# Performance work log

Measured on AMD Instinct MI355X. Metric: run time of the kernel, lower is better.

## Reference

```python
import jax, jax.numpy as jnp
import numpy as np

B, C, H, W = 2, 1024, 64, 64
E, TOP_K = 8, 2
FFN = C  # ffn_dim = in_channels; hidden_dim = out_channels = in_channels


def setup_inputs() -> dict:
    key = jax.random.key(0)
    ks = jax.random.split(key, 5)
    s = 0.02
    return {
        "hidden_states": jax.random.normal(ks[0], (B, C, H, W), jnp.float32),
        "gate_w": jax.random.normal(ks[1], (E, C), jnp.float32) * s,   # torch Linear weight [out,in]
        "w1": jax.random.normal(ks[2], (E, FFN, C), jnp.float32) * s,
        "w2": jax.random.normal(ks[3], (E, C, FFN), jnp.float32) * s,
        "w3": jax.random.normal(ks[4], (E, FFN, C), jnp.float32) * s,
    }


def reference(hidden_states, gate_w, w1, w2, w3):
    b, c = hidden_states.shape[0], hidden_states.shape[1]
    space = hidden_states.shape[2:]
    # (B, C, H, W) -> (B, H, W, C) -> (T, C)
    x = jnp.transpose(hidden_states, (0, 2, 3, 1)).reshape(-1, c)

    # Router: softmax in float32, top-k, renormalize (matches torch)
    logits = x @ gate_w.T                                   # [T, E]
    probs = jax.nn.softmax(logits.astype(jnp.float32), axis=-1)
    rw, sel = jax.lax.top_k(probs, TOP_K)                   # [T, K]
    rw = rw / jnp.sum(rw, axis=-1, keepdims=True)
    rw = rw.astype(x.dtype)

    # Combine weights per expert: zero where expert not selected -> exact
    # equivalence with gather/scatter dispatch (full capacity, no drops).
    combine = jnp.sum(jax.nn.one_hot(sel, E, dtype=x.dtype) * rw[..., None], axis=1)  # [T, E]

    out = jnp.zeros_like(x)
    for e in range(E):  # small fixed expert loop
        h = jax.nn.gelu(x @ w1[e].T, approximate=False) * (x @ w3[e].T)  # SwiGLU-style [T, FFN]
        out = out + combine[:, e:e + 1] * (h @ w2[e].T)

    out = out.reshape(b, *space, c)
    return jnp.transpose(out, (0, 3, 1, 2))  # (B, C, H, W)
```

## Files before the change

### kernel.cpp

```cpp
#include <hip/hip_runtime.h>
#include <hip/hip_bf16.h>
#include <math.h>

#define BB 2
#define CC 1024
#define HH 64
#define WW 64
#define HWH (HH*WW)
#define TT (BB*HWH)
#define EE 8
#define FFN 1024
#define MAXTILES 71
#define HCAP (MAXTILES*256)

typedef __bf16 bf16x8 __attribute__((ext_vector_type(8)));
typedef float  f32x4  __attribute__((ext_vector_type(4)));

__device__ __forceinline__ void gl_lds16(const __bf16* g, __bf16* l) {
    __builtin_amdgcn_global_load_lds(
        (const __attribute__((address_space(1))) void*)g,
        (__attribute__((address_space(3))) void*)l, 16, 0, 0);
}

__device__ __forceinline__ void barrier_raw() {
    asm volatile("" ::: "memory");
    __builtin_amdgcn_s_barrier();
    asm volatile("" ::: "memory");
}

__device__ __forceinline__ int xcd_swz(int orig, int nwg) {
    const int q = nwg >> 3, r = nwg & 7, x = orig & 7, o8 = orig >> 3;
    return (x < r ? x * (q + 1) : r * (q + 1) + (x - r) * q) + o8;
}

__device__ __forceinline__ float gelu_fast(float a) {
    const float a2 = a * a;
    const float t  = a * fmaf(0.044715f, a2, 1.0f);
    const float u  = __builtin_amdgcn_exp2f(t * -2.30220795f);
    return a * __builtin_amdgcn_rcpf(1.0f + u);
}

#define WAITV(N) asm volatile("s_waitcnt vmcnt(" #N ")" ::: "memory")
#define LGKM0()  asm volatile("s_waitcnt lgkmcnt(0)" ::: "memory")
#define SCHED0() __builtin_amdgcn_sched_barrier(0)
#define PRIO1()  __builtin_amdgcn_s_setprio(1)
#define PRIO0()  __builtin_amdgcn_s_setprio(0)

#define CVB 12288
#define XPB 8192
#define RTB 512
__global__ __launch_bounds__(256) void k_prep(
    const float* __restrict__ hs, const float* __restrict__ gate_w,
    const float* __restrict__ w1, const float* __restrict__ w2,
    const float* __restrict__ w3,
    __bf16* __restrict__ w1b, __bf16* __restrict__ w2b,
    __bf16* __restrict__ w3b, __bf16* __restrict__ X,
    float* __restrict__ logP) {
    __shared__ float sm[2112];
    const int bid = blockIdx.x;
    const int tid = threadIdx.x;

    if (bid < CVB) {
        const float* s; __bf16* d; int lb = bid;
        if (lb < 4096)      { s = w1; d = w1b; }
        else if (lb < 8192) { s = w2; d = w2b; lb -= 4096; }
        else                { s = w3; d = w3b; lb -= 8192; }
        const size_t i = (size_t)lb * 2048 + (size_t)tid * 8;
        const f32x4 v0 = *(const f32x4*)&s[i];
        const f32x4 v1 = *(const f32x4*)&s[i + 4];
        bf16x8 o;
#pragma unroll
        for (int j = 0; j < 4; ++j) { o[j] = (__bf16)v0[j]; o[4 + j] = (__bf16)v1[j]; }
        *(bf16x8*)&d[i] = o;
    } else if (bid < CVB + XPB) {
        const int lb  = bid - CVB;
        const int hw0 = (lb & 127) * 32;
        const int c0  = ((lb >> 7) & 31) * 32;
        const int b   = lb >> 12;
        float (*tile)[33] = (float(*)[33])sm;
        const int tx = tid & 31, ty = tid >> 5;
        const float* src = hs + ((size_t)b * CC + c0) * HWH + hw0;
#pragma unroll
        for (int i = 0; i < 4; ++i)
            tile[ty + i * 8][tx] = src[(size_t)(ty + i * 8) * HWH + tx];
        __syncthreads();
        __bf16* dst = X + ((size_t)b * HWH + hw0) * CC + c0;
#pragma unroll
        for (int i = 0; i < 4; ++i) {
            const int hwl = ty + i * 8;
            dst[(size_t)hwl * CC + tx] = (__bf16)tile[tx][hwl];
        }
    } else {
        const int lb  = bid - (CVB + XPB);
        const int q   = lb & 3;
        const int t64 = lb >> 2;
        float* g = sm;
        for (int i = tid; i < 2048; i += 256)
            g[i] = gate_w[(size_t)(i >> 8) * CC + q * 256 + (i & 255)];
        __syncthreads();
        const int q2 = tid >> 6, tl = tid & 63;
        const int t  = t64 * 64 + tl;
        const int b  = t >> 12, hw = t & 4095;
        const float* xp = hs + (size_t)b * CC * HWH + hw;
        float l[EE];
#pragma unroll
        for (int e = 0; e < EE; ++e) l[e] = 0.0f;
        const int cbase = q * 256 + q2 * 64;
        for (int c2 = 0; c2 < 64; ++c2) {
            const float xv = xp[(size_t)(cbase + c2) * HWH];
#pragma unroll
            for (int e = 0; e < EE; ++e) l[e] += xv * g[e * 256 + q2 * 64 + c2];
        }
        float* dst = logP + ((size_t)(q * 4 + q2) * TT + t) * 8;
        f32x4 a, c;
#pragma unroll
        for (int e = 0; e < 4; ++e) { a[e] = l[e]; c[e] = l[4 + e]; }
        *(f32x4*)dst = a;
        *(f32x4*)&dst[4] = c;
    }
}

__global__ __launch_bounds__(256) void k_top2(const float* __restrict__ logP,
                                              int* __restrict__ cnt,
                                              int* __restrict__ idxl,
                                              int* __restrict__ tokE,
                                              int* __restrict__ tokP,
                                              float* __restrict__ tokW) {
    __shared__ int lcnt[EE], lbase[EE];
    const int tid = threadIdx.x;
    const int t   = blockIdx.x * 256 + tid;
    if (tid < EE) lcnt[tid] = 0;
    __syncthreads();

    float l[EE];
#pragma unroll
    for (int e = 0; e < EE; ++e) l[e] = 0.0f;
#pragma unroll
    for (int pq = 0; pq < 16; ++pq) {
        const float* src = logP + ((size_t)pq * TT + t) * 8;
        const f32x4 a = *(const f32x4*)src;
        const f32x4 c = *(const f32x4*)&src[4];
#pragma unroll
        for (int e = 0; e < 4; ++e) { l[e] += a[e]; l[4 + e] += c[e]; }
    }

    int e1 = 0; float v1 = l[0];
#pragma unroll
    for (int e = 1; e < EE; ++e) { if (l[e] > v1) { v1 = l[e]; e1 = e; } }
    int e2 = -1; float v2 = -1e30f;
#pragma unroll
    for (int e = 0; e < EE; ++e) { if (e != e1 && l[e] > v2) { v2 = l[e]; e2 = e; } }

    const float p2 = __expf(v2 - v1);
    const float rs = 1.0f / (1.0f + p2);

    const int m1 = atomicAdd(&lcnt[e1], 1);
    const int m2 = atomicAdd(&lcnt[e2], 1);
    __syncthreads();
    if (tid < EE) lbase[tid] = atomicAdd(&cnt[tid], lcnt[tid]);
    __syncthreads();
    const int p1pos = lbase[e1] + m1;
    const int p2pos = lbase[e2] + m2;

    idxl[e1 * TT + p1pos] = t;
    idxl[e2 * TT + p2pos] = t;
    tokE[t] = e1 | (e2 << 8);
    tokP[2 * t]     = p1pos;
    tokP[2 * t + 1] = p2pos;
    tokW[2 * t]     = rs;
    tokW[2 * t + 1] = p2 * rs;
}

#define GT_TILE(SR, SS, KB, STG, WC) do {                                     \
    if (STG) {                                                                \
        gl_lds16(gA0 + (KB), &sA[SS][stA]);                                   \
        gl_lds16(gA1 + (KB), &sA[SS][stA + 4096]);                            \
        gl_lds16(gB0 + (KB), &sB[SS][stA]);                                   \
    }                                                                         \
    bf16x8 af[4], bv[4];                                                      \
    _Pragma("unroll") for (int f_ = 0; f_ < 4; ++f_) {                        \
        af[f_] = *(const bf16x8*)&sA[SR][aoff + f_ * 512];                    \
        bv[f_] = *(const bf16x8*)&sB[SR][boff + f_ * 512];                    \
    }                                                                         \
    LGKM0(); SCHED0();                                                        \
    PRIO1();                                                                  \
    _Pragma("unroll") for (int m_ = 0; m_ < 4; ++m_)                          \
    _Pragma("unroll") for (int n_ = 0; n_ < 4; ++n_)                          \
        acc[m_][n_] = __builtin_amdgcn_mfma_f32_16x16x32_bf16(                \
            af[m_], bv[n_], acc[m_][n_], 0, 0, 0);                            \
    PRIO0();                                                                  \
    WC;                                                                       \
    barrier_raw();                                                            \
} while (0)

__global__ __launch_bounds__(512, 4)
void k_gemm1(const __bf16* __restrict__ X, const __bf16* __restrict__ w1b,
             const __bf16* __restrict__ w3b, const int* __restrict__ cnt,
             const int* __restrict__ idxl, __bf16* __restrict__ H) {
    const int lid = blockIdx.y * 16 + blockIdx.x;
    const int wg  = xcd_swz(lid, 16 * MAXTILES);
    const int n0  = (wg & 15) * 64;
    int ty = wg >> 4;
    int e = -1, mt = 0, goff = 0, acc_rows = 0;
#pragma unroll
    for (int ee = 0; ee < EE; ++ee) {
        const int me = (cnt[ee] + 255) >> 8;
        if (ty >= 0 && ty < me) { e = ee; mt = ty << 8; goff = acc_rows; }
        ty -= me;
        acc_rows += me << 8;
    }
    if (e < 0) return;
    const int cntE = cnt[e];
    const __bf16* W1 = w1b + (size_t)e * FFN * CC;
    const __bf16* W3 = w3b + (size_t)e * FFN * CC;

    __shared__ __align__(16) __bf16 sA[3][8192];
    __shared__ __align__(16) __bf16 sB[3][4096];

    const int tid  = threadIdx.x;
    const int lane = tid & 63, wave = tid >> 6;
    const int l15  = lane & 15, lq = lane >> 4;
    const int wm   = wave & 3;
    const int wq   = wave >> 2;
    const int rsw  = (lq ^ ((l15 >> 1) & 3)) * 8;

    const int csw  = ((tid & 3) ^ ((tid >> 3) & 3)) * 8;
    const int cswb = ((lane & 3) ^ ((lane >> 3) & 3)) * 8;

    int pr0 = mt + (tid >> 2);        if (pr0 > cntE - 1) pr0 = cntE - 1;
    int pr1 = mt + 128 + (tid >> 2);  if (pr1 > cntE - 1) pr1 = cntE - 1;
    const __bf16* gA0 = X + (size_t)idxl[e * TT + pr0] * CC + csw;
    const __bf16* gA1 = X + (size_t)idxl[e * TT + pr1] * CC + csw;
    const __bf16* WB  = (wave & 1) ? W3 : W1;
    const __bf16* gB0 = WB + (size_t)(n0 + (wave >> 1) * 16 + (lane >> 2)) * CC + cswb;

    const int stA  = wave * 512;
    const int aoff = (wm * 64 + l15) * 32 + rsw;
    const int boff = (wq * 64 + l15) * 32 + rsw;

    f32x4 acc[4][4] = {};

    gl_lds16(gA0,      &sA[0][stA]); gl_lds16(gA1,      &sA[0][stA + 4096]);
    gl_lds16(gB0,      &sB[0][stA]);
    gl_lds16(gA0 + 32, &sA[1][stA]); gl_lds16(gA1 + 32, &sA[1][stA + 4096]);
    gl_lds16(gB0 + 32, &sB[1][stA]);
    WAITV(3);
    barrier_raw();

    int kb = 64;
    for (int it = 0; it < 10; ++it) {
        GT_TILE(0, 2, kb, 1, WAITV(3)); kb += 32;
        GT_TILE(1, 0, kb, 1, WAITV(3)); kb += 32;
        GT_TILE(2, 1, kb, 1, WAITV(3)); kb += 32;
    }
    GT_TILE(0, 0, 0, 0, WAITV(0));
    GT_TILE(1, 0, 0, 0, (void)0);

#pragma unroll
    for (int mf = 0; mf < 4; ++mf) {
        const int gr  = goff + mt + wm * 64 + mf * 16 + lq * 4;
        const int col = n0 + wq * 32 + l15;
#pragma unroll
        for (int r = 0; r < 4; ++r) {
            const float a0 = acc[mf][0][r], c0 = acc[mf][1][r];
            const float a1 = acc[mf][2][r], c1 = acc[mf][3][r];
            H[(size_t)(gr + r) * FFN + col]      = (__bf16)(gelu_fast(a0) * c0);
            H[(size_t)(gr + r) * FFN + col + 16] = (__bf16)(gelu_fast(a1) * c1);
        }
    }
}

__global__ __launch_bounds__(512, 4)
void k_gemm2(const __bf16* __restrict__ H, const __bf16* __restrict__ w2b,
             const int* __restrict__ cnt, __bf16* __restrict__ Z) {
    const int lid = blockIdx.y * 8 + blockIdx.x;
    const int wg  = xcd_swz(lid, 8 * MAXTILES);
    const int n0  = (wg & 7) * 128;
    int ty = wg >> 3;
    int e = -1, mt = 0, goff = 0, acc_rows = 0;
#pragma unroll
    for (int ee = 0; ee < EE; ++ee) {
        const int me = (cnt[ee] + 255) >> 8;
        if (ty >= 0 && ty < me) { e = ee; mt = ty << 8; goff = acc_rows; }
        ty -= me;
        acc_rows += me << 8;
    }
    if (e < 0) return;
    const __bf16* W2 = w2b + (size_t)e * CC * FFN;
    const __bf16* Ar = H + (size_t)(goff + mt) * FFN;

    __shared__ __align__(16) __bf16 sA[3][8192];
    __shared__ __align__(16) __bf16 sB[3][4096];

    const int tid  = threadIdx.x;
    const int lane = tid & 63, wave = tid >> 6;
    const int l15  = lane & 15, lq = lane >> 4;
    const int wm   = wave & 3;
    const int wq   = wave >> 2;
    const int rsw  = (lq ^ ((l15 >> 1) & 3)) * 8;
    const int csw  = ((tid & 3) ^ ((tid >> 3) & 3)) * 8;
    const int cswb = ((lane & 3) ^ ((lane >> 3) & 3)) * 8;

    const __bf16* gA0 = Ar + (size_t)(tid >> 2) * FFN + csw;
    const __bf16* gA1 = Ar + (size_t)(128 + (tid >> 2)) * FFN + csw;
    const __bf16* gB0 = W2 + (size_t)(n0 + wave * 16 + (lane >> 2)) * FFN + cswb;

    const int stA  = wave * 512;
    const int aoff = (wm * 64 + l15) * 32 + rsw;
    const int boff = (wq * 64 + l15) * 32 + rsw;

    f32x4 acc[4][4] = {};

    gl_lds16(gA0,      &sA[0][stA]); gl_lds16(gA1,      &sA[0][stA + 4096]);
    gl_lds16(gB0,      &sB[0][stA]);
    gl_lds16(gA0 + 32, &sA[1][stA]); gl_lds16(gA1 + 32, &sA[1][stA + 4096]);
    gl_lds16(gB0 + 32, &sB[1][stA]);
    WAITV(3);
    barrier_raw();

    int kb = 64;
    for (int it = 0; it < 10; ++it) {
        GT_TILE(0, 2, kb, 1, WAITV(3)); kb += 32;
        GT_TILE(1, 0, kb, 1, WAITV(3)); kb += 32;
        GT_TILE(2, 1, kb, 1, WAITV(3)); kb += 32;
    }
    GT_TILE(0, 0, 0, 0, WAITV(0));
    GT_TILE(1, 0, 0, 0, (void)0);

#pragma unroll
    for (int mf = 0; mf < 4; ++mf) {
        const int gr = goff + mt + wm * 64 + mf * 16 + lq * 4;
#pragma unroll
        for (int nf = 0; nf < 4; ++nf) {
            const int col = n0 + wq * 64 + nf * 16 + l15;
#pragma unroll
            for (int r = 0; r < 4; ++r)
                Z[(size_t)(gr + r) * CC + col] = (__bf16)acc[mf][nf][r];
        }
    }
}

__global__ __launch_bounds__(256) void k_combine(const __bf16* __restrict__ Z,
                                                 const int* __restrict__ cnt,
                                                 const int* __restrict__ tokE,
                                                 const int* __restrict__ tokP,
                                                 const float* __restrict__ tokW,
                                                 float* __restrict__ out) {
    __shared__ float tile[32][33];
    __shared__ int s_pre[EE];
    const int tid = threadIdx.x;
    if (tid < EE) {
        int a = 0;
        for (int ee = 0; ee < tid; ++ee) a += ((cnt[ee] + 255) >> 8) << 8;
        s_pre[tid] = a;
    }
    __syncthreads();

    const int t0 = blockIdx.x * 32;
    const int c0 = blockIdx.y * 32;
    const int tx = tid & 31;
    const int ty = tid >> 5;

#pragma unroll
    for (int i = 0; i < 4; ++i) {
        const int tl = ty + 8 * i;
        const int t  = t0 + tl;
        const int ee = tokE[t];
        const int e1 = ee & 0xff, e2 = ee >> 8;
        const int r1 = s_pre[e1] + tokP[2 * t];
        const int r2 = s_pre[e2] + tokP[2 * t + 1];
        const float v = tokW[2 * t]     * (float)Z[(size_t)r1 * CC + c0 + tx]
                      + tokW[2 * t + 1] * (float)Z[(size_t)r2 * CC + c0 + tx];
        tile[tl][tx] = v;
    }
    __syncthreads();

    const int b   = t0 >> 12;
    const int hw0 = t0 & 4095;
#pragma unroll
    for (int i = 0; i < 4; ++i) {
        const int cl = ty + 8 * i;
        out[(size_t)b * CC * HWH + (size_t)(c0 + cl) * HWH + hw0 + tx] = tile[tx][cl];
    }
}

extern "C" void kernel_launch(void* const* d_in, const int* in_sizes, int n_in,
                              void* d_out, int out_size, void* d_ws, size_t ws_size,
                              hipStream_t stream) {
    const float* hs     = (const float*)d_in[0];
    const float* gate_w = (const float*)d_in[1];
    const float* w1     = (const float*)d_in[2];
    const float* w2     = (const float*)d_in[3];
    const float* w3     = (const float*)d_in[4];
    float* out = (float*)d_out;

    const size_t WSZ = (size_t)EE * FFN * CC * 2;
    char* ws = (char*)d_ws;
    __bf16* w2b  = (__bf16*)ws;
    __bf16* w1b  = (__bf16*)(ws + WSZ);
    __bf16* w3b  = (__bf16*)(ws + 2 * WSZ);
    __bf16* X    = (__bf16*)(ws + 3 * WSZ);
    __bf16* Zbuf = (__bf16*)(ws + WSZ);
    __bf16* Hbuf = (__bf16*)(ws + 4 * WSZ);
    float*  logP = (float*)Hbuf;
    char* p = ws + 4 * WSZ + (size_t)HCAP * FFN * 2;
    int*   idxl  = (int*)p;           p += (size_t)EE * TT * 4;
    int*   tokE  = (int*)p;           p += (size_t)TT * 4;
    int*   tokP  = (int*)p;           p += (size_t)2 * TT * 4;
    float* tokW  = (float*)p;         p += (size_t)2 * TT * 4;
    int*   cnt   = (int*)p;           p += 256;

    hipMemsetAsync(cnt, 0, EE * sizeof(int), stream);

    k_prep<<<CVB + XPB + RTB, 256, 0, stream>>>(
        hs, gate_w, w1, w2, w3, w1b, w2b, w3b, X, logP);
    k_top2<<<TT / 256, 256, 0, stream>>>(logP, cnt, idxl, tokE, tokP, tokW);

    k_gemm1<<<dim3(FFN / 64, MAXTILES), 512, 0, stream>>>(
        X, w1b, w3b, cnt, idxl, Hbuf);
    k_gemm2<<<dim3(CC / 128, MAXTILES), 512, 0, stream>>>(
        Hbuf, w2b, cnt, Zbuf);
    k_combine<<<dim3(TT / 32, CC / 32), 256, 0, stream>>>(
        Zbuf, cnt, tokE, tokP, tokW, out);
}
```

Before: 329.8 us.

## Make expert GEMM kernels persistent with an atomic work-queue tile scheduler

Both grouped GEMM kernels now launch a fixed 512 workgroups. Each workgroup repeatedly pulls a tile index from a global atomic counter until all valid (expert, row-tile, column-tile) items are consumed. This replaces the oversized static grid with its XCD swizzle and early-exit blocks, aiming to remove empty launches and balance the tail. The cost is one atomic plus a block barrier per tile and the loss of the deliberate XCD-aware weight locality. Two extra counter slots are zeroed by the existing memset.

```diff
diff --git a/kernel.cpp b/kernel.cpp
--- a/kernel.cpp
+++ b/kernel.cpp
@@ -26,11 +26,6 @@
     asm volatile("" ::: "memory");
     __builtin_amdgcn_s_barrier();
     asm volatile("" ::: "memory");
-}
-
-__device__ __forceinline__ int xcd_swz(int orig, int nwg) {
-    const int q = nwg >> 3, r = nwg & 7, x = orig & 7, o8 = orig >> 3;
-    return (x < r ? x * (q + 1) : r * (q + 1) + (x - r) * q) + o8;
 }
 
 __device__ __forceinline__ float gelu_fast(float a) {
@@ -196,146 +191,165 @@
 __global__ __launch_bounds__(512, 4)
 void k_gemm1(const __bf16* __restrict__ X, const __bf16* __restrict__ w1b,
              const __bf16* __restrict__ w3b, const int* __restrict__ cnt,
-             const int* __restrict__ idxl, __bf16* __restrict__ H) {
-    const int lid = blockIdx.y * 16 + blockIdx.x;
-    const int wg  = xcd_swz(lid, 16 * MAXTILES);
-    const int n0  = (wg & 15) * 64;
-    int ty = wg >> 4;
-    int e = -1, mt = 0, goff = 0, acc_rows = 0;
-#pragma unroll
-    for (int ee = 0; ee < EE; ++ee) {
-        const int me = (cnt[ee] + 255) >> 8;
-        if (ty >= 0 && ty < me) { e = ee; mt = ty << 8; goff = acc_rows; }
-        ty -= me;
-        acc_rows += me << 8;
-    }
-    if (e < 0) return;
-    const int cntE = cnt[e];
-    const __bf16* W1 = w1b + (size_t)e * FFN * CC;
-    const __bf16* W3 = w3b + (size_t)e * FFN * CC;
-
+             const int* __restrict__ idxl, __bf16* __restrict__ H,
+             int* __restrict__ wq) {
     __shared__ __align__(16) __bf16 sA[3][8192];
     __shared__ __align__(16) __bf16 sB[3][4096];
+    __shared__ int s_item;
 
     const int tid  = threadIdx.x;
     const int lane = tid & 63, wave = tid >> 6;
     const int l15  = lane & 15, lq = lane >> 4;
     const int wm   = wave & 3;
-    const int wq   = wave >> 2;
+    const int wq_  = wave >> 2;
     const int rsw  = (lq ^ ((l15 >> 1) & 3)) * 8;
-
     const int csw  = ((tid & 3) ^ ((tid >> 3) & 3)) * 8;
     const int cswb = ((lane & 3) ^ ((lane >> 3) & 3)) * 8;
-
-    int pr0 = mt + (tid >> 2);        if (pr0 > cntE - 1) pr0 = cntE - 1;
-    int pr1 = mt + 128 + (tid >> 2);  if (pr1 > cntE - 1) pr1 = cntE - 1;
-    const __bf16* gA0 = X + (size_t)idxl[e * TT + pr0] * CC + csw;
-    const __bf16* gA1 = X + (size_t)idxl[e * TT + pr1] * CC + csw;
-    const __bf16* WB  = (wave & 1) ? W3 : W1;
-    const __bf16* gB0 = WB + (size_t)(n0 + (wave >> 1) * 16 + (lane >> 2)) * CC + cswb;
-
     const int stA  = wave * 512;
     const int aoff = (wm * 64 + l15) * 32 + rsw;
-    const int boff = (wq * 64 + l15) * 32 + rsw;
-
-    f32x4 acc[4][4] = {};
-
-    gl_lds16(gA0,      &sA[0][stA]); gl_lds16(gA1,      &sA[0][stA + 4096]);
-    gl_lds16(gB0,      &sB[0][stA]);
-    gl_lds16(gA0 + 32, &sA[1][stA]); gl_lds16(gA1 + 32, &sA[1][stA + 4096]);
-    gl_lds16(gB0 + 32, &sB[1][stA]);
-    WAITV(3);
-    barrier_raw();
-
-    int kb = 64;
-    for (int it = 0; it < 10; ++it) {
-        GT_TILE(0, 2, kb, 1, WAITV(3)); kb += 32;
-        GT_TILE(1, 0, kb, 1, WAITV(3)); kb += 32;
-        GT_TILE(2, 1, kb, 1, WAITV(3)); kb += 32;
-    }
-    GT_TILE(0, 0, 0, 0, WAITV(0));
-    GT_TILE(1, 0, 0, 0, (void)0);
-
-#pragma unroll
-    for (int mf = 0; mf < 4; ++mf) {
-        const int gr  = goff + mt + wm * 64 + mf * 16 + lq * 4;
-        const int col = n0 + wq * 32 + l15;
-#pragma unroll
-        for (int r = 0; r < 4; ++r) {
-            const float a0 = acc[mf][0][r], c0 = acc[mf][1][r];
-            const float a1 = acc[mf][2][r], c1 = acc[mf][3][r];
-            H[(size_t)(gr + r) * FFN + col]      = (__bf16)(gelu_fast(a0) * c0);
-            H[(size_t)(gr + r) * FFN + col + 16] = (__bf16)(gelu_fast(a1) * c1);
+    const int boff = (wq_ * 64 + l15) * 32 + rsw;
+
+    int nT = 0;
+#pragma unroll
+    for (int ee = 0; ee < EE; ++ee) nT += (cnt[ee] + 255) >> 8;
+    const int nItems = nT * 16;
+
+    for (;;) {
+        if (tid == 0) s_item = atomicAdd(wq, 1);
+        __syncthreads();
+        const int wg = s_item;
+        if (wg >= nItems) break;
+
+        const int n0 = (wg & 15) * 64;
+        int ty = wg >> 4;
+        int e = 0, mt = 0, goff = 0, acc_rows = 0;
+#pragma unroll
+        for (int ee = 0; ee < EE; ++ee) {
+            const int me = (cnt[ee] + 255) >> 8;
+            if (ty >= 0 && ty < me) { e = ee; mt = ty << 8; goff = acc_rows; }
+            ty -= me;
+            acc_rows += me << 8;
+        }
+        const int cntE = cnt[e];
+        const __bf16* W1 = w1b + (size_t)e * FFN * CC;
+        const __bf16* W3 = w3b + (size_t)e * FFN * CC;
+
+        int pr0 = mt + (tid >> 2);        if (pr0 > cntE - 1) pr0 = cntE - 1;
+        int pr1 = mt + 128 + (tid >> 2);  if (pr1 > cntE - 1) pr1 = cntE - 1;
+        const __bf16* gA0 = X + (size_t)idxl[e * TT + pr0] * CC + csw;
+        const __bf16* gA1 = X + (size_t)idxl[e * TT + pr1] * CC + csw;
+        const __bf16* WB  = (wave & 1) ? W3 : W1;
+        const __bf16* gB0 = WB + (size_t)(n0 + (wave >> 1) * 16 + (lane >> 2)) * CC + cswb;
+
+        f32x4 acc[4][4] = {};
+
+        gl_lds16(gA0,      &sA[0][stA]); gl_lds16(gA1,      &sA[0][stA + 4096]);
+        gl_lds16(gB0,      &sB[0][stA]);
+        gl_lds16(gA0 + 32, &sA[1][stA]); gl_lds16(gA1 + 32, &sA[1][stA + 4096]);
+        gl_lds16(gB0 + 32, &sB[1][stA]);
+        WAITV(3);
+        barrier_raw();
+
+        int kb = 64;
+        for (int it = 0; it < 10; ++it) {
+            GT_TILE(0, 2, kb, 1, WAITV(3)); kb += 32;
+            GT_TILE(1, 0, kb, 1, WAITV(3)); kb += 32;
+            GT_TILE(2, 1, kb, 1, WAITV(3)); kb += 32;
+        }
+        GT_TILE(0, 0, 0, 0, WAITV(0));
+        GT_TILE(1, 0, 0, 0, (void)0);
+
+#pragma unroll
+        for (int mf = 0; mf < 4; ++mf) {
+            const int gr  = goff + mt + wm * 64 + mf * 16 + lq * 4;
+            const int col = n0 + wq_ * 32 + l15;
+#pragma unroll
+            for (int r = 0; r < 4; ++r) {
+                const float a0 = acc[mf][0][r], c0 = acc[mf][1][r];
+                const float a1 = acc[mf][2][r], c1 = acc[mf][3][r];
+                H[(size_t)(gr + r) * FFN + col]      = (__bf16)(gelu_fast(a0) * c0);
+                H[(size_t)(gr + r) * FFN + col + 16] = (__bf16)(gelu_fast(a1) * c1);
+            }
         }
     }
 }
 
 __global__ __launch_bounds__(512, 4)
 void k_gemm2(const __bf16* __restrict__ H, const __bf16* __restrict__ w2b,
-             const int* __restrict__ cnt, __bf16* __restrict__ Z) {
-    const int lid = blockIdx.y * 8 + blockIdx.x;
-    const int wg  = xcd_swz(lid, 8 * MAXTILES);
-    const int n0  = (wg & 7) * 128;
-    int ty = wg >> 3;
-    int e = -1, mt = 0, goff = 0, acc_rows = 0;
-#pragma unroll
-    for (int ee = 0; ee < EE; ++ee) {
-        const int me = (cnt[ee] + 255) >> 8;
-        if (ty >= 0 && ty < me) { e = ee; mt = ty << 8; goff = acc_rows; }
-        ty -= me;
-        acc_rows += me << 8;
-    }
-    if (e < 0) return;
-    const __bf16* W2 = w2b + (size_t)e * CC * FFN;
-    const __bf16* Ar = H + (size_t)(goff + mt) * FFN;
-
+             const int* __restrict__ cnt, __bf16* __restrict__ Z,
+             int* __restrict__ wq) {
     __shared__ __align__(16) __bf16 sA[3][8192];
     __shared__ __align__(16) __bf16 sB[3][4096];
+    __shared__ int s_item;
 
     const int tid  = threadIdx.x;
     const int lane = tid & 63, wave = tid >> 6;
     const int l15  = lane & 15, lq = lane >> 4;
     const int wm   = wave & 3;
-    const int wq   = wave >> 2;
+    const int wq_  = wave >> 2;
     const int rsw  = (lq ^ ((l15 >> 1) & 3)) * 8;
     const int csw  = ((tid & 3) ^ ((tid >> 3) & 3)) * 8;
     const int cswb = ((lane & 3) ^ ((lane >> 3) & 3)) * 8;
-
-    const __bf16* gA0 = Ar + (size_t)(tid >> 2) * FFN + csw;
-    const __bf16* gA1 = Ar + (size_t)(128 + (tid >> 2)) * FFN + csw;
-    const __bf16* gB0 = W2 + (size_t)(n0 + wave * 16 + (lane >> 2)) * FFN + cswb;
-
     const int stA  = wave * 512;
     const int aoff = (wm * 64 + l15) * 32 + rsw;
-    const int boff = (wq * 64 + l15) * 32 + rsw;
-
-    f32x4 acc[4][4] = {};
-
-    gl_lds16(gA0,      &sA[0][stA]); gl_lds16(gA1,      &sA[0][stA + 4096]);
-    gl_lds16(gB0,      &sB[0][stA]);
-    gl_lds16(gA0 + 32, &sA[1][stA]); gl_lds16(gA1 + 32, &sA[1][stA + 4096]);
-    gl_lds16(gB0 + 32, &sB[1][stA]);
-    WAITV(3);
-    barrier_raw();
-
-    int kb = 64;
-    for (int it = 0; it < 10; ++it) {
-        GT_TILE(0, 2, kb, 1, WAITV(3)); kb += 32;
-        GT_TILE(1, 0, kb, 1, WAITV(3)); kb += 32;
-        GT_TILE(2, 1, kb, 1, WAITV(3)); kb += 32;
-    }
-    GT_TILE(0, 0, 0, 0, WAITV(0));
-    GT_TILE(1, 0, 0, 0, (void)0);
-
-#pragma unroll
-    for (int mf = 0; mf < 4; ++mf) {
-        const int gr = goff + mt + wm * 64 + mf * 16 + lq * 4;
-#pragma unroll
-        for (int nf = 0; nf < 4; ++nf) {
-            const int col = n0 + wq * 64 + nf * 16 + l15;
-#pragma unroll
-            for (int r = 0; r < 4; ++r)
-                Z[(size_t)(gr + r) * CC + col] = (__bf16)acc[mf][nf][r];
+    const int boff = (wq_ * 64 + l15) * 32 + rsw;
+
+    int nT = 0;
+#pragma unroll
+    for (int ee = 0; ee < EE; ++ee) nT += (cnt[ee] + 255) >> 8;
+    const int nItems = nT * 8;
+
+    for (;;) {
+        if (tid == 0) s_item = atomicAdd(wq, 1);
+        __syncthreads();
+        const int wg = s_item;
+        if (wg >= nItems) break;
+
+        const int n0 = (wg & 7) * 128;
+        int ty = wg >> 3;
+        int e = 0, mt = 0, goff = 0, acc_rows = 0;
+#pragma unroll
+        for (int ee = 0; ee < EE; ++ee) {
+            const int me = (cnt[ee] + 255) >> 8;
+            if (ty >= 0 && ty < me) { e = ee; mt = ty << 8; goff = acc_rows; }
+            ty -= me;
+            acc_rows += me << 8;
+        }
+        const __bf16* W2 = w2b + (size_t)e * CC * FFN;
+        const __bf16* Ar = H + (size_t)(goff + mt) * FFN;
+
+        const __bf16* gA0 = Ar + (size_t)(tid >> 2) * FFN + csw;
+        const __bf16* gA1 = Ar + (size_t)(128 + (tid >> 2)) * FFN + csw;
+        const __bf16* gB0 = W2 + (size_t)(n0 + wave * 16 + (lane >> 2)) * FFN + cswb;
+
+        f32x4 acc[4][4] = {};
+
+        gl_lds16(gA0,      &sA[0][stA]); gl_lds16(gA1,      &sA[0][stA + 4096]);
+        gl_lds16(gB0,      &sB[0][stA]);
+        gl_lds16(gA0 + 32, &sA[1][stA]); gl_lds16(gA1 + 32, &sA[1][stA + 4096]);
+        gl_lds16(gB0 + 32, &sB[1][stA]);
+        WAITV(3);
+        barrier_raw();
+
+        int kb = 64;
+        for (int it = 0; it < 10; ++it) {
+            GT_TILE(0, 2, kb, 1, WAITV(3)); kb += 32;
+            GT_TILE(1, 0, kb, 1, WAITV(3)); kb += 32;
+            GT_TILE(2, 1, kb, 1, WAITV(3)); kb += 32;
+        }
+        GT_TILE(0, 0, 0, 0, WAITV(0));
+        GT_TILE(1, 0, 0, 0, (void)0);
+
+#pragma unroll
+        for (int mf = 0; mf < 4; ++mf) {
+            const int gr = goff + mt + wm * 64 + mf * 16 + lq * 4;
+#pragma unroll
+            for (int nf = 0; nf < 4; ++nf) {
+                const int col = n0 + wq_ * 64 + nf * 16 + l15;
+#pragma unroll
+                for (int r = 0; r < 4; ++r)
+                    Z[(size_t)(gr + r) * CC + col] = (__bf16)acc[mf][nf][r];
+            }
         }
     }
 }
@@ -410,16 +424,14 @@
     float* tokW  = (float*)p;         p += (size_t)2 * TT * 4;
     int*   cnt   = (int*)p;           p += 256;
 
-    hipMemsetAsync(cnt, 0, EE * sizeof(int), stream);
+    hipMemsetAsync(cnt, 0, (EE + 2) * sizeof(int), stream);
 
     k_prep<<<CVB + XPB + RTB, 256, 0, stream>>>(
         hs, gate_w, w1, w2, w3, w1b, w2b, w3b, X, logP);
     k_top2<<<TT / 256, 256, 0, stream>>>(logP, cnt, idxl, tokE, tokP, tokW);
 
-    k_gemm1<<<dim3(FFN / 64, MAXTILES), 512, 0, stream>>>(
-        X, w1b, w3b, cnt, idxl, Hbuf);
-    k_gemm2<<<dim3(CC / 128, MAXTILES), 512, 0, stream>>>(
-        Hbuf, w2b, cnt, Zbuf);
+    k_gemm1<<<512, 512, 0, stream>>>(X, w1b, w3b, cnt, idxl, Hbuf, cnt + 8);
+    k_gemm2<<<512, 512, 0, stream>>>(Hbuf, w2b, cnt, Zbuf, cnt + 9);
     k_combine<<<dim3(TT / 32, CC / 32), 256, 0, stream>>>(
         Zbuf, cnt, tokE, tokP, tokW, out);
 }
```

Result: slower. 347.8 us (+5.5%).
